# Optimization experiments

Measured on AMD Instinct MI355X. Metric: run time of the kernel, lower is better.

Reference implementation:

```python
import jax, jax.numpy as jnp
import numpy as np

HID = 512
EMB = 345
SEQ = 512


def _lstm_dir(x, Wih, Whh, b, reverse):
    # x: (S, in), Wih: (4H, in), Whh: (4H, H), b: (4H,)  [torch gate order i,f,g,o]
    H = Whh.shape[1]
    zin = x @ Wih.T + b  # precompute input contribution: (S, 4H)

    def step(carry, z):
        h, c = carry
        z = z + h @ Whh.T
        i, f, g, o = jnp.split(z, 4)
        c = jax.nn.sigmoid(f) * c + jax.nn.sigmoid(i) * jnp.tanh(g)
        h = jax.nn.sigmoid(o) * jnp.tanh(c)
        return (h, c), h

    init = (jnp.zeros((H,), x.dtype), jnp.zeros((H,), x.dtype))
    _, hs = jax.lax.scan(step, init, zin, reverse=reverse)
    return hs  # (S, H), time-aligned for both directions


def _bilstm(x, Wih0, Whh0, b0, Wih_r, Whh_r, b_r):
    out = jnp.concatenate([
        _lstm_dir(x, Wih0[0], Whh0[0], b0[0], False),
        _lstm_dir(x, Wih0[1], Whh0[1], b0[1], True)], axis=-1)
    for l in range(Wih_r.shape[0]):  # remaining 3 stacked layers
        out = jnp.concatenate([
            _lstm_dir(out, Wih_r[l, 0], Whh_r[l, 0], b_r[l, 0], False),
            _lstm_dir(out, Wih_r[l, 1], Whh_r[l, 1], b_r[l, 1], True)], axis=-1)
    return out  # (S, 2H)


def setup_inputs() -> dict:
    key = jax.random.key(0)
    ks = jax.random.split(key, 16)
    H4, H2 = 4 * HID, 2 * HID
    s = 0.05
    x = jax.random.normal(ks[0], (SEQ, EMB), jnp.float32)
    heads = jax.random.randint(ks[1], (SEQ + 1,), 0, SEQ + 1)
    heads = heads.at[0].set(-1)  # root has no head
    Wih0 = jax.random.normal(ks[2], (2, H4, EMB), jnp.float32) * s
    Whh0 = jax.random.normal(ks[3], (2, H4, HID), jnp.float32) * s
    b0 = jax.random.normal(ks[4], (2, H4), jnp.float32) * s
    Wih_r = jax.random.normal(ks[5], (3, 2, H4, H2), jnp.float32) * s
    Whh_r = jax.random.normal(ks[6], (3, 2, H4, HID), jnp.float32) * s
    b_r = jax.random.normal(ks[7], (3, 2, H4), jnp.float32) * s
    W1 = jax.random.normal(ks[8], (256, 2 * H2), jnp.float32) * s
    b1 = jax.random.normal(ks[9], (256,), jnp.float32) * s
    W2 = jax.random.normal(ks[10], (128, 256), jnp.float32) * s
    b2 = jax.random.normal(ks[11], (128,), jnp.float32) * s
    W3 = jax.random.normal(ks[12], (64, 128), jnp.float32) * s
    b3 = jax.random.normal(ks[13], (64,), jnp.float32) * s
    W4 = jax.random.normal(ks[14], (1, 64), jnp.float32) * s
    b4 = jax.random.normal(ks[15], (1,), jnp.float32) * s
    return dict(x=x, heads=heads, Wih0=Wih0, Whh0=Whh0, b0=b0,
                Wih_r=Wih_r, Whh_r=Whh_r, b_r=b_r,
                W1=W1, b1=b1, W2=W2, b2=b2, W3=W3, b3=b3, W4=W4, b4=b4)


def reference(x, heads, Wih0, Whh0, b0, Wih_r, Whh_r, b_r,
              W1, b1, W2, b2, W3, b3, W4, b4):
    lstm_out = _bilstm(x, Wih0, Whh0, b0, Wih_r, Whh_r, b_r)  # (S, 2H)
    H2 = lstm_out.shape[-1]
    avail = jnp.concatenate([jnp.zeros((1, H2), x.dtype), lstm_out], axis=0)  # (N, 2H)
    N = avail.shape[0]
    # network(cat(w1, w2)) split: W1 acts on the two halves independently
    A = avail @ W1[:, :H2].T  # (N, 256)
    B = avail @ W1[:, H2:].T  # (N, 256)
    h1 = jax.nn.relu(A[:, None, :] + B[None, :, :] + b1)  # (N, N, 256)
    h2 = jax.nn.relu(h1 @ W2.T + b2)                       # (N, N, 128)
    h3 = jax.nn.relu(h2 @ W3.T + b3)                       # (N, N, 64)
    S = (h3 @ W4.T + b4)[..., 0]                           # (N, N) raw scores
    T = jnp.where(jnp.arange(N)[None, :] == heads[:, None], 100.0, 0.0)
    loss = jnp.sum((S - T) ** 2) / (N * N)  # sum of per-pair MSE / N^2
    probs = jax.nn.softmax(S, axis=1)  # scipy softmax(score_matrix, axis=1)
    return loss, probs
```

## Files before the change

### kernel.cpp

```cpp
#include <hip/hip_runtime.h>
#include <math.h>

#define HID 512
#define SEQ 512
#define EMB 345
#define NN  513
#define MPAD 576
#define H4  2048
#define H2  1024

__global__ __launch_bounds__(256)
void gemm_nt(const float* __restrict__ A, int lda, long aStride,
             const float* __restrict__ B, int ldb, long bStride,
             const float* __restrict__ bias, long biasStride,
             float* __restrict__ C, int ldc, long cStride, int K)
{
    int z = blockIdx.z;
    A += (long)z * aStride; B += (long)z * bStride; C += (long)z * cStride;
    const float* bptr = bias ? bias + (long)z * biasStride : nullptr;
    __shared__ float As[16][68];
    __shared__ float Bs[16][68];
    int tid = threadIdx.x;
    int tx = tid & 15, ty = tid >> 4;
    int m0 = blockIdx.y * 64, n0 = blockIdx.x * 64;
    float acc[4][4] = {};
    for (int k0 = 0; k0 < K; k0 += 16) {
        #pragma unroll
        for (int i = 0; i < 4; i++) {
            int id = tid + 256 * i;
            int mn = id >> 4, kk = id & 15;
            int k = k0 + kk;
            As[kk][mn] = (k < K) ? A[(long)(m0 + mn) * lda + k] : 0.f;
            Bs[kk][mn] = (k < K) ? B[(long)(n0 + mn) * ldb + k] : 0.f;
        }
        __syncthreads();
        #pragma unroll
        for (int kk = 0; kk < 16; kk++) {
            float a[4], b[4];
            #pragma unroll
            for (int i = 0; i < 4; i++) a[i] = As[kk][ty * 4 + i];
            #pragma unroll
            for (int j = 0; j < 4; j++) b[j] = Bs[kk][tx * 4 + j];
            #pragma unroll
            for (int i = 0; i < 4; i++)
                #pragma unroll
                for (int j = 0; j < 4; j++) acc[i][j] += a[i] * b[j];
        }
        __syncthreads();
    }
    #pragma unroll
    for (int i = 0; i < 4; i++) {
        int m = m0 + ty * 4 + i;
        #pragma unroll
        for (int j = 0; j < 4; j++) {
            int n = n0 + tx * 4 + j;
            float v = acc[i][j];
            if (bptr) v += bptr[n];
            C[(long)m * ldc + n] = v;
        }
    }
}

__device__ __forceinline__ float sigmf(float x) { return 1.f / (1.f + __expf(-x)); }

__global__ __launch_bounds__(256, 1)
void lstm_layer(const float* __restrict__ zin,
                const float* __restrict__ Whh,
                float* out)
{
    int wg  = blockIdx.x;
    int dir = wg >> 5;
    int kb  = (wg & 31) * 16;
    int tid = threadIdx.x;
    int r = tid & 63;
    int p = tid >> 6;
    int gate = r >> 4;
    int kq = r & 15;
    long row = (long)gate * 512 + kb + kq;

    __shared__ float h_lds[512];
    __shared__ float part[256];
    __shared__ float rowsum[64];

    float4 wreg[32];
    const float4* wp = (const float4*)(Whh + ((long)dir * H4 + row) * HID + p * 128);
    #pragma unroll
    for (int j = 0; j < 32; j++) wreg[j] = wp[j];

    const float* zin_d = zin + (long)dir * SEQ * H4;
    float c_st = 0.f;
    int lane = tid & 63;

    for (int t = 0; t < SEQ; t++) {
        int at = (dir == 0) ? t : (SEQ - 1 - t);
        float z0 = 0.f, z1 = 0.f, z2 = 0.f, z3 = 0.f;
        if (tid < 16) {
            const float* zp = zin_d + (long)at * H4 + kb + tid;
            z0 = zp[0]; z1 = zp[512]; z2 = zp[1024]; z3 = zp[1536];
        }
        if (t == 0) {
            h_lds[tid] = 0.f; h_lds[tid + 256] = 0.f;
        } else if (lane < 32) {
            int at_prev = (dir == 0) ? (t - 1) : (SEQ - t);
            const unsigned long long* src =
                (const unsigned long long*)(out + (long)at_prev * H2 + dir * HID + p * 128)
                + lane * 2;
            unsigned long long a = __hip_atomic_load(src,     __ATOMIC_RELAXED, __HIP_MEMORY_SCOPE_AGENT);
            unsigned long long b = __hip_atomic_load(src + 1, __ATOMIC_RELAXED, __HIP_MEMORY_SCOPE_AGENT);
            while (((unsigned)a == 0xFFFFFFFFu) | ((unsigned)(a >> 32) == 0xFFFFFFFFu) |
                   ((unsigned)b == 0xFFFFFFFFu) | ((unsigned)(b >> 32) == 0xFFFFFFFFu)) {
                __builtin_amdgcn_s_sleep(1);
                a = __hip_atomic_load(src,     __ATOMIC_RELAXED, __HIP_MEMORY_SCOPE_AGENT);
                b = __hip_atomic_load(src + 1, __ATOMIC_RELAXED, __HIP_MEMORY_SCOPE_AGENT);
            }
            union { unsigned long long u[2]; float4 f; } cv;
            cv.u[0] = a; cv.u[1] = b;
            *(float4*)&h_lds[p * 128 + lane * 4] = cv.f;
        }
        __syncthreads();
        const float4* h4 = (const float4*)(h_lds + p * 128);
        float4 av = {0.f, 0.f, 0.f, 0.f};
        #pragma unroll
        for (int j = 0; j < 32; j++) {
            float4 w = wreg[j], h = h4[j];
            av.x += w.x * h.x; av.y += w.y * h.y;
            av.z += w.z * h.z; av.w += w.w * h.w;
        }
        part[tid] = (av.x + av.y) + (av.z + av.w);
        __syncthreads();
        if (tid < 64) rowsum[tid] = part[tid] + part[tid + 64] + part[tid + 128] + part[tid + 192];
        __syncthreads();
        if (tid < 16) {
            float zi = z0 + rowsum[tid];
            float zf = z1 + rowsum[16 + tid];
            float zg = z2 + rowsum[32 + tid];
            float zo = z3 + rowsum[48 + tid];
            float cc = sigmf(zf) * c_st + sigmf(zi) * tanhf(zg);
            c_st = cc;
            float hh = sigmf(zo) * tanhf(cc);
            __hip_atomic_store(out + (long)at * H2 + dir * HID + kb + tid, hh,
                               __ATOMIC_RELAXED, __HIP_MEMORY_SCOPE_AGENT);
        }
    }
}

__global__ __launch_bounds__(256)
void build_avail(const float* __restrict__ lstm_out, float* __restrict__ avail)
{
    long idx = (long)blockIdx.x * 256 + threadIdx.x;
    if (idx >= (long)MPAD * H2) return;
    int i = (int)(idx >> 10);
    int c = (int)(idx & 1023);
    float v = 0.f;
    if (i >= 1 && i <= SEQ) v = lstm_out[(long)(i - 1) * H2 + c];
    avail[idx] = v;
}

__global__ __launch_bounds__(256)
void transpose_w(const float* __restrict__ W, float* __restrict__ WT, int rows, int cols)
{
    int idx = blockIdx.x * 256 + threadIdx.x;
    if (idx >= rows * cols) return;
    int rr = idx / cols, cc = idx % cols;
    WT[cc * rows + rr] = W[idx];
}

#define STR1 257
#define STR2 129
__global__ __launch_bounds__(256)
void pair_kernel(const float* __restrict__ Abuf, const float* __restrict__ Bbuf,
                 const float* __restrict__ b1, const float* __restrict__ W2T,
                 const float* __restrict__ b2, const float* __restrict__ W3T,
                 const float* __restrict__ b3, const float* __restrict__ W4,
                 const float* __restrict__ b4, float* __restrict__ S)
{
    __shared__ float At[8 * STR1];
    __shared__ float Bt[8 * STR1];
    __shared__ float b1s[256];
    __shared__ float h2s[64 * STR2];
    __shared__ float spart[4 * 64];
    int tid = threadIdx.x;
    int i0 = blockIdx.y * 8, j0 = blockIdx.x * 8;
    {
        int rr = tid >> 5;
        int cbase = (tid & 31) * 8;
        #pragma unroll
        for (int u = 0; u < 8; u++) {
            At[rr * STR1 + cbase + u] = Abuf[(long)(i0 + rr) * 256 + cbase + u];
            Bt[rr * STR1 + cbase + u] = Bbuf[(long)(j0 + rr) * 256 + cbase + u];
        }
        b1s[tid] = b1[tid];
    }
    __syncthreads();
    int w = tid >> 6;
    int lane = tid & 63;
    int ii = lane >> 3, jj = lane & 7;
    #pragma unroll 1
    for (int blk = 0; blk < 4; blk++) {
        int c2b = __builtin_amdgcn_readfirstlane(w * 32 + blk * 8);
        float acc[8] = {};
        #pragma unroll 4
        for (int c1 = 0; c1 < 256; c1++) {
            float h1v = At[ii * STR1 + c1] + Bt[jj * STR1 + c1] + b1s[c1];
            h1v = fmaxf(h1v, 0.f);
            const float* wrow = W2T + c1 * 128 + c2b;
            #pragma unroll
            for (int u = 0; u < 8; u++) acc[u] += wrow[u] * h1v;
        }
        #pragma unroll
        for (int u = 0; u < 8; u++)
            h2s[lane * STR2 + c2b + u] = fmaxf(acc[u] + b2[c2b + u], 0.f);
    }
    __syncthreads();
    float sp = 0.f;
    #pragma unroll 1
    for (int blk = 0; blk < 2; blk++) {
        int c3b = __builtin_amdgcn_readfirstlane(w * 16 + blk * 8);
        float acc[8] = {};
        #pragma unroll 4
        for (int c2 = 0; c2 < 128; c2++) {
            float h2v = h2s[lane * STR2 + c2];
            const float* wrow = W3T + c2 * 64 + c3b;
            #pragma unroll
            for (int u = 0; u < 8; u++) acc[u] += wrow[u] * h2v;
        }
        #pragma unroll
        for (int u = 0; u < 8; u++) {
            float v = fmaxf(acc[u] + b3[c3b + u], 0.f);
            sp += W4[c3b + u] * v;
        }
    }
    spart[w * 64 + lane] = sp;
    __syncthreads();
    if (tid < 64) {
        float s = spart[tid] + spart[64 + tid] + spart[128 + tid] + spart[192 + tid] + b4[0];
        int i = i0 + (tid >> 3), j = j0 + (tid & 7);
        if (i < NN && j < NN) S[(long)i * NN + j] = s;
    }
}

__global__ __launch_bounds__(256)
void softmax_row(const float* __restrict__ S, const int* __restrict__ heads,
                 float* __restrict__ probs, float* __restrict__ rowloss)
{
    int i = blockIdx.x;
    int tid = threadIdx.x;
    __shared__ float red[256];
    __shared__ float srow[NN];
    const float* Si = S + (long)i * NN;
    float mx = -1e30f;
    for (int j = tid; j < NN; j += 256) { float v = Si[j]; srow[j] = v; mx = fmaxf(mx, v); }
    red[tid] = mx; __syncthreads();
    for (int s = 128; s > 0; s >>= 1) { if (tid < s) red[tid] = fmaxf(red[tid], red[tid + s]); __syncthreads(); }
    mx = red[0]; __syncthreads();
    float sum = 0.f, sq = 0.f;
    int hd = heads[i];
    for (int j = tid; j < NN; j += 256) {
        float v = srow[j];
        sum += __expf(v - mx);
        float t = (j == hd) ? 100.f : 0.f;
        float d = v - t; sq += d * d;
    }
    red[tid] = sum; __syncthreads();
    for (int s = 128; s > 0; s >>= 1) { if (tid < s) red[tid] += red[tid + s]; __syncthreads(); }
    sum = red[0]; __syncthreads();
    red[tid] = sq; __syncthreads();
    for (int s = 128; s > 0; s >>= 1) { if (tid < s) red[tid] += red[tid + s]; __syncthreads(); }
    if (tid == 0) rowloss[i] = red[0];
    float inv = 1.f / sum;
    for (int j = tid; j < NN; j += 256) probs[(long)i * NN + j] = __expf(srow[j] - mx) * inv;
}

__global__ __launch_bounds__(256)
void finish_loss(const float* __restrict__ rowloss, float* __restrict__ out0)
{
    __shared__ float red[256];
    int tid = threadIdx.x;
    float s = 0.f;
    for (int i = tid; i < NN; i += 256) s += rowloss[i];
    red[tid] = s; __syncthreads();
    for (int k = 128; k > 0; k >>= 1) { if (tid < k) red[tid] += red[tid + k]; __syncthreads(); }
    if (tid == 0) out0[0] = red[0] / ((float)NN * (float)NN);
}

extern "C" void kernel_launch(void* const* d_in, const int* in_sizes, int n_in,
                              void* d_out, int out_size, void* d_ws, size_t ws_size,
                              hipStream_t stream)
{
    const float* x     = (const float*)d_in[0];
    const int*   heads = (const int*)  d_in[1];
    const float* Wih0  = (const float*)d_in[2];
    const float* Whh0  = (const float*)d_in[3];
    const float* b0    = (const float*)d_in[4];
    const float* Wih_r = (const float*)d_in[5];
    const float* Whh_r = (const float*)d_in[6];
    const float* b_r   = (const float*)d_in[7];
    const float* W1    = (const float*)d_in[8];
    const float* b1    = (const float*)d_in[9];
    const float* W2    = (const float*)d_in[10];
    const float* b2    = (const float*)d_in[11];
    const float* W3    = (const float*)d_in[12];
    const float* b3    = (const float*)d_in[13];
    const float* W4    = (const float*)d_in[14];
    const float* b4    = (const float*)d_in[15];
    float* out = (float*)d_out;

    char* ws = (char*)d_ws;
    const size_t o_zin  = 0;
    const size_t o_outA = o_zin  + (size_t)2 * SEQ * H4 * 4 + 512;
    const size_t o_outB = o_outA + (size_t)SEQ * H2 * 4 + 512;
    const size_t o_avail= o_outB + (size_t)SEQ * H2 * 4 + 512;
    const size_t o_Abuf = o_avail+ (size_t)MPAD * H2 * 4 + 512;
    const size_t o_Bbuf = o_Abuf + (size_t)MPAD * 256 * 4 + 512;
    const size_t o_W2T  = o_Bbuf + (size_t)MPAD * 256 * 4 + 512;
    const size_t o_W3T  = o_W2T  + 256 * 128 * 4 + 512;
    const size_t o_S    = o_W3T  + 128 * 64 * 4 + 512;
    const size_t o_rl   = o_S    + (size_t)NN * NN * 4 + 512;

    float* zin   = (float*)(ws + o_zin);
    float* outA  = (float*)(ws + o_outA);
    float* outB  = (float*)(ws + o_outB);
    float* avail = (float*)(ws + o_avail);
    float* Abuf  = (float*)(ws + o_Abuf);
    float* Bbuf  = (float*)(ws + o_Bbuf);
    float* W2T   = (float*)(ws + o_W2T);
    float* W3T   = (float*)(ws + o_W3T);
    float* Sbuf  = (float*)(ws + o_S);
    float* rowl  = (float*)(ws + o_rl);

    const size_t outBytes = (size_t)SEQ * H2 * 4;

    gemm_nt<<<dim3(H4 / 64, SEQ / 64, 2), 256, 0, stream>>>(
        x, EMB, 0, Wih0, EMB, (long)H4 * EMB, b0, H4,
        zin, H4, (long)SEQ * H4, EMB);
    hipMemsetAsync(outA, 0xFF, outBytes, stream);
    lstm_layer<<<64, 256, 0, stream>>>(zin, Whh0, outA);

    float* bufs[2] = { outA, outB };
    for (int l = 1; l <= 3; l++) {
        const float* src = bufs[(l - 1) & 1];
        float* dst = bufs[l & 1];
        gemm_nt<<<dim3(H4 / 64, SEQ / 64, 2), 256, 0, stream>>>(
            src, H2, 0, Wih_r + (size_t)(l - 1) * 2 * H4 * H2, H2, (long)H4 * H2,
            b_r + (size_t)(l - 1) * 2 * H4, H4,
            zin, H4, (long)SEQ * H4, H2);
        hipMemsetAsync(dst, 0xFF, outBytes, stream);
        lstm_layer<<<64, 256, 0, stream>>>(
            zin, Whh_r + (size_t)(l - 1) * 2 * H4 * HID, dst);
    }
    float* lstm_final = bufs[3 & 1];

    build_avail<<<(MPAD * H2) / 256, 256, 0, stream>>>(lstm_final, avail);

    gemm_nt<<<dim3(256 / 64, MPAD / 64, 1), 256, 0, stream>>>(
        avail, H2, 0, W1, 2048, 0, nullptr, 0, Abuf, 256, 0, H2);
    gemm_nt<<<dim3(256 / 64, MPAD / 64, 1), 256, 0, stream>>>(
        avail, H2, 0, W1 + 1024, 2048, 0, nullptr, 0, Bbuf, 256, 0, H2);

    transpose_w<<<(128 * 256) / 256, 256, 0, stream>>>(W2, W2T, 128, 256);
    transpose_w<<<(64 * 128) / 256, 256, 0, stream>>>(W3, W3T, 64, 128);

    pair_kernel<<<dim3(65, 65), 256, 0, stream>>>(
        Abuf, Bbuf, b1, W2T, b2, W3T, b3, W4, b4, Sbuf);

    softmax_row<<<NN, 256, 0, stream>>>(Sbuf, heads, out + 1, rowl);
    finish_loss<<<1, 256, 0, stream>>>(rowl, out);
}
```

Measured before the change: 5.499 ms.

## Cut per-step LSTM barriers with wave-private h slices and shuffle reduction

Each wavefront now polls and loads only the 128-element slice of the previous hidden state that it consumes, into its own LDS region, so no block barrier is needed before the matvec. The partial-sum buffer is double-buffered by timestep parity. The cross-row reduction is done by wave 0 with lane shuffles instead of an extra LDS array and two more barriers, leaving one __syncthreads per step instead of three. The gate math also switches to hardware reciprocal and an exp-based tanh, which trades a little accuracy for shorter latency on the serial critical path.

New measurement: 4.805 ms. 1.14x faster.

```diff
diff --git a/kernel.cpp b/kernel.cpp
--- a/kernel.cpp
+++ b/kernel.cpp
@@ -61,7 +61,10 @@
     }
 }
 
-__device__ __forceinline__ float sigmf(float x) { return 1.f / (1.f + __expf(-x)); }
+__device__ __forceinline__ float sigmf(float x)
+{ return __builtin_amdgcn_rcpf(1.f + __expf(-x)); }
+__device__ __forceinline__ float tanhf_fast(float x)
+{ return 1.f - 2.f * __builtin_amdgcn_rcpf(1.f + __expf(2.f * x)); }
 
 __global__ __launch_bounds__(256, 1)
 void lstm_layer(const float* __restrict__ zin,
@@ -72,15 +75,14 @@
     int dir = wg >> 5;
     int kb  = (wg & 31) * 16;
     int tid = threadIdx.x;
-    int r = tid & 63;
+    int lane = tid & 63;
     int p = tid >> 6;
-    int gate = r >> 4;
-    int kq = r & 15;
+    int gate = lane >> 4;
+    int kq = lane & 15;
     long row = (long)gate * 512 + kb + kq;
 
     __shared__ float h_lds[512];
-    __shared__ float part[256];
-    __shared__ float rowsum[64];
+    __shared__ float part[2][256];
 
     float4 wreg[32];
     const float4* wp = (const float4*)(Whh + ((long)dir * H4 + row) * HID + p * 128);
@@ -89,7 +91,9 @@
 
     const float* zin_d = zin + (long)dir * SEQ * H4;
     float c_st = 0.f;
-    int lane = tid & 63;
+
+    h_lds[p * 128 + lane] = 0.f;
+    h_lds[p * 128 + 64 + lane] = 0.f;
 
     for (int t = 0; t < SEQ; t++) {
         int at = (dir == 0) ? t : (SEQ - 1 - t);
@@ -98,26 +102,20 @@
             const float* zp = zin_d + (long)at * H4 + kb + tid;
             z0 = zp[0]; z1 = zp[512]; z2 = zp[1024]; z3 = zp[1536];
         }
-        if (t == 0) {
-            h_lds[tid] = 0.f; h_lds[tid + 256] = 0.f;
-        } else if (lane < 32) {
+        if (t > 0) {
             int at_prev = (dir == 0) ? (t - 1) : (SEQ - t);
             const unsigned long long* src =
                 (const unsigned long long*)(out + (long)at_prev * H2 + dir * HID + p * 128)
-                + lane * 2;
-            unsigned long long a = __hip_atomic_load(src,     __ATOMIC_RELAXED, __HIP_MEMORY_SCOPE_AGENT);
-            unsigned long long b = __hip_atomic_load(src + 1, __ATOMIC_RELAXED, __HIP_MEMORY_SCOPE_AGENT);
-            while (((unsigned)a == 0xFFFFFFFFu) | ((unsigned)(a >> 32) == 0xFFFFFFFFu) |
-                   ((unsigned)b == 0xFFFFFFFFu) | ((unsigned)(b >> 32) == 0xFFFFFFFFu)) {
+                + lane;
+            unsigned long long a = __hip_atomic_load(src, __ATOMIC_RELAXED, __HIP_MEMORY_SCOPE_AGENT);
+            while (((unsigned)a == 0xFFFFFFFFu) | ((unsigned)(a >> 32) == 0xFFFFFFFFu)) {
                 __builtin_amdgcn_s_sleep(1);
-                a = __hip_atomic_load(src,     __ATOMIC_RELAXED, __HIP_MEMORY_SCOPE_AGENT);
-                b = __hip_atomic_load(src + 1, __ATOMIC_RELAXED, __HIP_MEMORY_SCOPE_AGENT);
+                a = __hip_atomic_load(src, __ATOMIC_RELAXED, __HIP_MEMORY_SCOPE_AGENT);
             }
-            union { unsigned long long u[2]; float4 f; } cv;
-            cv.u[0] = a; cv.u[1] = b;
-            *(float4*)&h_lds[p * 128 + lane * 4] = cv.f;
-        }
-        __syncthreads();
+            union { unsigned long long u; float2 f; } cv;
+            cv.u = a;
+            *(float2*)&h_lds[p * 128 + lane * 2] = cv.f;
+        }
         const float4* h4 = (const float4*)(h_lds + p * 128);
         float4 av = {0.f, 0.f, 0.f, 0.f};
         #pragma unroll
@@ -126,20 +124,25 @@
             av.x += w.x * h.x; av.y += w.y * h.y;
             av.z += w.z * h.z; av.w += w.w * h.w;
         }
-        part[tid] = (av.x + av.y) + (av.z + av.w);
+        part[t & 1][tid] = (av.x + av.y) + (av.z + av.w);
         __syncthreads();
-        if (tid < 64) rowsum[tid] = part[tid] + part[tid + 64] + part[tid + 128] + part[tid + 192];
-        __syncthreads();
-        if (tid < 16) {
-            float zi = z0 + rowsum[tid];
-            float zf = z1 + rowsum[16 + tid];
-            float zg = z2 + rowsum[32 + tid];
-            float zo = z3 + rowsum[48 + tid];
-            float cc = sigmf(zf) * c_st + sigmf(zi) * tanhf(zg);
-            c_st = cc;
-            float hh = sigmf(zo) * tanhf(cc);
-            __hip_atomic_store(out + (long)at * H2 + dir * HID + kb + tid, hh,
-                               __ATOMIC_RELAXED, __HIP_MEMORY_SCOPE_AGENT);
+        if (p == 0) {
+            const float* pb = part[t & 1];
+            float rs = pb[lane] + pb[lane + 64] + pb[lane + 128] + pb[lane + 192];
+            float rf = __shfl(rs, (lane & 15) + 16);
+            float rg = __shfl(rs, (lane & 15) + 32);
+            float ro = __shfl(rs, (lane & 15) + 48);
+            if (lane < 16) {
+                float zi = z0 + rs;
+                float zf = z1 + rf;
+                float zg = z2 + rg;
+                float zo = z3 + ro;
+                float cc = sigmf(zf) * c_st + sigmf(zi) * tanhf_fast(zg);
+                c_st = cc;
+                float hh = sigmf(zo) * tanhf_fast(cc);
+                __hip_atomic_store(out + (long)at * H2 + dir * HID + kb + lane, hh,
+                                   __ATOMIC_RELAXED, __HIP_MEMORY_SCOPE_AGENT);
+            }
         }
     }
 }
```
